# Performance work log

Hardware: AMD Instinct MI355X
Metric: run time of the kernel (lower is better)

Reference implementation:

```python
import jax, jax.numpy as jnp
import numpy as np

N = 2000
E = 20000
C = 16
B = 128
N_IN = 200   # first N_IN nodes are input nodes
N_OUT = 200  # last N_OUT nodes are output nodes
EPS = 1e-5


def setup_inputs() -> dict:
    key = jax.random.key(0)
    ks = jax.random.split(key, 8)
    x = jax.random.normal(ks[0], (B, N), dtype=jnp.float32)
    edge_index = jax.random.randint(ks[1], (2, E), 0, N, dtype=jnp.int32)
    input_node_mask = jnp.arange(N) < N_IN
    output_node_mask = jnp.arange(N) >= (N - N_OUT)
    func_mask = ~(input_node_mask | output_node_mask)
    # sparse-linear parameters (structured forms of W1/W2/W3)
    w1 = jax.random.normal(ks[2], (E, C), dtype=jnp.float32) * (1.0 / np.sqrt(C))
    b1 = jnp.zeros((N, C), dtype=jnp.float32)
    w2 = jax.random.normal(ks[3], (N, C, C), dtype=jnp.float32) * (1.0 / np.sqrt(C))
    b2 = jnp.zeros((N, C), dtype=jnp.float32)
    w3 = jax.random.normal(ks[4], (E, C), dtype=jnp.float32) * 1.0  # d=1 init scale
    b3 = jnp.zeros((E,), dtype=jnp.float32)
    g1 = jnp.ones((N * C,), dtype=jnp.float32)
    be1 = jnp.zeros((N * C,), dtype=jnp.float32)
    g2 = jnp.ones((N * C,), dtype=jnp.float32)
    be2 = jnp.zeros((N * C,), dtype=jnp.float32)
    return {"x": x, "w1": w1, "b1": b1, "w2": w2, "b2": b2, "w3": w3, "b3": b3,
            "g1": g1, "be1": be1, "g2": g2, "be2": be2,
            "edge_index": edge_index, "func_mask": func_mask,
            "output_node_mask": output_node_mask, "layers": 4}


def _batchnorm(h, g, b):
    # training-mode BatchNorm1d: batch mean and biased variance over axis 0
    m = h.mean(axis=0)
    v = h.var(axis=0)
    return (h - m) * jax.lax.rsqrt(v + EPS) * g + b


def reference(x, w1, b1, w2, b2, w3, b3, g1, be1, g2, be2,
              edge_index, func_mask, output_node_mask, layers):
    src, dst = edge_index[0], edge_index[1]
    Bsz, Nn = x.shape
    Ee, Cc = w1.shape
    fm = func_mask.astype(x.dtype)
    w2m = w2 * fm[:, None, None]          # W2 blocks exist only at function nodes
    w3m = w3 * fm[src][:, None]           # W3 rows exist only for edges with src in function nodes

    x0 = x[:, src]                        # node2edge: (B, E)
    xe = x0
    for _ in range(layers):
        # lin1: scatter edge values into dst node hidden channels
        contrib = xe.T[:, :, None] * w1[:, None, :]                    # (E, B, C)
        h = jax.ops.segment_sum(contrib, dst, num_segments=Nn)         # (N, B, C)
        h = jnp.transpose(h, (1, 0, 2)) + b1                           # (B, N, C)
        h = _batchnorm(h.reshape(Bsz, Nn * Cc), g1, be1)
        h = jax.nn.elu(h).reshape(Bsz, Nn, Cc)
        # lin2: block-diagonal C x C mix per (function) node
        h = jnp.einsum('bnc,ncd->bnd', h, w2m) + b2
        h = _batchnorm(h.reshape(Bsz, Nn * Cc), g2, be2)
        h = jax.nn.elu(h).reshape(Bsz, Nn, Cc)
        # lin3: gather src hidden, per-edge dot back to edge space
        xe = jnp.einsum('bec,ec->be', h[:, src], w3m) + b3             # (B, E)
        xe = xe + x0
    # edge2node: scatter-sum edge values to dst nodes, keep output nodes
    nodes = jax.ops.segment_sum(xe.T, dst, num_segments=Nn)            # (N, B)
    return nodes.T * output_node_mask.astype(x.dtype)
```

## Files before the change

kernel.cpp:

```cpp
#include <hip/hip_runtime.h>
#include <math.h>

#define BB 128
#define NN 2000
#define EE 20000
#define CC 16
#define FUNC_LO 200
#define FUNC_HI 1800
#define OUT_LO 1800
#define NFUNC 1600
#define NBLK 1600
#define EPSV 1e-5f
#define SS 40
#define NSLOT (NFUNC * SS)
#define HP 129

#define SCOPE_AGENT __HIP_MEMORY_SCOPE_AGENT

static __device__ __forceinline__ void xe_st(float* p, float v) {
    __hip_atomic_store(p, v, __ATOMIC_RELAXED, SCOPE_AGENT);
}

__device__ __forceinline__ void arrive(int* progress, int L) {
    asm volatile("s_waitcnt vmcnt(0)" ::: "memory");
    __syncthreads();
    if (threadIdx.x == 0)
        __hip_atomic_store(&progress[blockIdx.x], L, __ATOMIC_RELAXED, SCOPE_AGENT);
}

__device__ __forceinline__ void wait_producers(const int* progress,
                                               const int* __restrict__ pblk,
                                               int cbase, int dIn, int L) {
    if (threadIdx.x < 64) {
        int j = threadIdx.x;
        int pb = (j < dIn) ? pblk[cbase + j] : -1;
        bool done = (pb < 0);
        int tries = 0;
        while (true) {
            if (!done)
                done = (__hip_atomic_load(&progress[pb], __ATOMIC_RELAXED,
                                          SCOPE_AGENT) >= L);
            if (__ballot(!done) == 0ull) break;
            __builtin_amdgcn_s_sleep(2);
            if (++tries > (1 << 18)) break;
        }
    }
    __syncthreads();
}

#define TPB0 100
__global__ void k_prep(const float* __restrict__ x, const int* __restrict__ ei,
                       const float* __restrict__ w1, const float* __restrict__ w3,
                       const float* __restrict__ b3,
                       int* __restrict__ degIn, int* __restrict__ degF,
                       int* __restrict__ degO, int* __restrict__ posIn,
                       float* __restrict__ xT, float* __restrict__ w1s,
                       float* __restrict__ w3s, float* __restrict__ b3s,
                       int* __restrict__ inoff, int* __restrict__ wout,
                       int* __restrict__ prodBlk, float* __restrict__ out)
{
    int t = blockIdx.x * 256 + threadIdx.x;
    if (t < EE) {
        int s = ei[t], d = ei[EE + t];
        bool dFn = (d >= FUNC_LO && d < FUNC_HI);
        bool sFn = (s >= FUNC_LO && s < FUNC_HI);
        int pi = -1;
        if (dFn) {
            int p = atomicAdd(&degIn[d], 1);
            pi = (d - FUNC_LO) * SS + p;
            posIn[t] = pi;
            const float4* w1v = (const float4*)w1 + (size_t)t * 4;
            float4* w1o = (float4*)w1s + (size_t)pi * 4;
            #pragma unroll
            for (int i = 0; i < 4; i++) w1o[i] = w1v[i];
            inoff[pi] = s * BB;
            prodBlk[pi] = sFn ? (s - FUNC_LO) : (t % NBLK);
        }
        if (sFn) {
            int po = -1;
            if (dFn) {
                int q = atomicAdd(&degF[s], 1);
                po = (s - FUNC_LO) * SS + q;
                wout[po] = pi * BB;
            } else if (d >= OUT_LO) {
                int q = atomicAdd(&degO[s], 1);
                po = (s - FUNC_LO) * SS + (SS - 1 - q);
                wout[po] = d;
            }
            if (po >= 0) {
                const float4* w3v = (const float4*)w3 + (size_t)t * 4;
                float4* w3o = (float4*)w3s + (size_t)po * 4;
                #pragma unroll
                for (int i = 0; i < 4; i++) w3o[i] = w3v[i];
                b3s[po] = b3[t];
            }
        }
    }
    if (t < NN * BB) out[t] = 0.0f;

    int tb = blockIdx.x - TPB0;
    if (tb >= 0 && tb < 63 * 4) {
        __shared__ float tl[32][33];
        int ntile = tb >> 2, btile = tb & 3;
        int n0 = ntile * 32, b0 = btile * 32;
        int tx = threadIdx.x & 31, ty = threadIdx.x >> 5;
        #pragma unroll
        for (int r = 0; r < 4; r++) {
            int bb = b0 + ty * 4 + r;
            int nn2 = n0 + tx;
            tl[ty * 4 + r][tx] = (nn2 < NN) ? x[(size_t)bb * NN + nn2] : 0.0f;
        }
        __syncthreads();
        #pragma unroll
        for (int r = 0; r < 4; r++) {
            int nn2 = n0 + ty * 4 + r;
            if (nn2 < NN) xT[(size_t)nn2 * BB + b0 + tx] = tl[tx][ty * 4 + r];
        }
    }
}

__device__ __forceinline__ void bn_elu(float (&t)[CC],
                                       const float* g, const float* be,
                                       float* tile, float* part_s, float* part_ss,
                                       float* sc, float* sh, int b) {
    #pragma unroll
    for (int c = 0; c < CC; c++) tile[c * HP + b] = t[c];
    __syncthreads();
    {
        int c = b & 15, grp = b >> 4;
        float s = 0.f, ss = 0.f;
        #pragma unroll
        for (int i = 0; i < 16; i++) {
            float v = tile[c * HP + grp * 16 + i];
            s += v; ss += v * v;
        }
        part_s[grp * 16 + c] = s;
        part_ss[grp * 16 + c] = ss;
    }
    __syncthreads();
    if (b < CC) {
        float S = 0.f, SSm = 0.f;
        #pragma unroll
        for (int g8 = 0; g8 < 8; g8++) { S += part_s[g8 * 16 + b]; SSm += part_ss[g8 * 16 + b]; }
        float mean = S * (1.0f / BB);
        float var = SSm * (1.0f / BB) - mean * mean;
        float scale = rsqrtf(var + EPSV) * g[b];
        sc[b] = scale;
        sh[b] = be[b] - mean * scale;
    }
    __syncthreads();
    #pragma unroll
    for (int c = 0; c < CC; c++) {
        float u = t[c] * sc[c] + sh[c];
        t[c] = (u > 0.0f) ? u : (__expf(u) - 1.0f);
    }
}

struct FusedArgs {
    const float* xT; float* xeA; float* xeB; float* xeC;
    const float* w1s; const float* w2; const float* w3s; const float* b3s;
    const int* inoff; const int* wout; const int* prodBlk;
    const int* degIn; const int* degF; const int* degO;
    const float* g1; const float* be1; const float* g2; const float* be2;
    const int* ei; const int* posIn; const float* b3;
    float* out;
    int* progress;
};

template<bool FIRST, bool LAST>
__device__ __forceinline__ void layer_body(const FusedArgs& A,
    const float* __restrict__ xe_in, float* __restrict__ xe_out,
    int n, int b, int dIn, int dF, int dO, float x0r,
    const float* w1L, const float* w3L, const float* w2L, const float* b3L,
    const int* ioL, const int* woL,
    const float* g1L, const float* be1L, const float* g2L, const float* be2L,
    float* tile, float* part_s, float* part_ss, float* sc, float* sh)
{
    float a[CC];
    #pragma unroll
    for (int c = 0; c < CC; c++) a[c] = 0.0f;

    for (int k0 = 0; k0 < dIn; k0 += 16) {
        float v[16];
        #pragma unroll
        for (int j = 0; j < 16; j++) {
            v[j] = 0.0f;
            if (k0 + j < dIn) {
                int ro = FIRST ? ioL[k0 + j] : (k0 + j) * BB;
                v[j] = xe_in[ro + b];
            }
        }
        #pragma unroll
        for (int j = 0; j < 16; j++) {
            if (k0 + j < dIn) {
                const float* wr = &w1L[(k0 + j) * CC];
                #pragma unroll
                for (int c = 0; c < CC; c++) a[c] += v[j] * wr[c];
            }
        }
    }

    bn_elu(a, g1L, be1L, tile, part_s, part_ss, sc, sh, b);

    float h2[CC];
    #pragma unroll
    for (int d = 0; d < CC; d++) h2[d] = 0.0f;
    #pragma unroll
    for (int c = 0; c < CC; c++) {
        float av = a[c];
        #pragma unroll
        for (int d = 0; d < CC; d++) h2[d] += av * w2L[c * CC + d];
    }

    bn_elu(h2, g2L, be2L, tile, part_s, part_ss, sc, sh, b);

    if (!LAST) {
        for (int q0 = 0; q0 < dF; q0 += 4) {
            #pragma unroll
            for (int j = 0; j < 4; j++) {
                int q = q0 + j;
                if (q >= dF) break;
                const float* wr = &w3L[q * CC];
                float val = b3L[q] + x0r;
                #pragma unroll
                for (int d = 0; d < CC; d++) val += h2[d] * wr[d];
                xe_st(&xe_out[woL[q] + b], val);
            }
        }
    } else {
        for (int q0 = 0; q0 < dO; q0 += 4) {
            #pragma unroll
            for (int j = 0; j < 4; j++) {
                int q = q0 + j;
                if (q >= dO) break;
                int ql = SS - 1 - q;
                const float* wr = &w3L[ql * CC];
                float val = b3L[ql] + x0r;
                #pragma unroll
                for (int d = 0; d < CC; d++) val += h2[d] * wr[d];
                int dn = woL[ql];
                atomicAdd(&A.out[(size_t)b * NN + dn], val);
            }
        }
    }
}

__global__ __launch_bounds__(128, 4) void k_fused(FusedArgs A)
{
    const int b = threadIdx.x;
    const int blk = blockIdx.x;
    const int n = FUNC_LO + blk;
    const int cbase = blk * SS;

    __shared__ float tile[CC * HP];
    __shared__ float part_s[128], part_ss[128];
    __shared__ float sc[CC], sh[CC];
    __shared__ float w1L[SS * CC];
    __shared__ float w3L[SS * CC];
    __shared__ float w2L[CC * CC];
    __shared__ float b3L[SS];
    __shared__ int   ioL[SS];
    __shared__ int   woL[SS];
    __shared__ float g1L[CC], be1L[CC], g2L[CC], be2L[CC];

    #pragma unroll
    for (int i = b; i < SS * CC; i += 128) {
        w1L[i] = A.w1s[(size_t)cbase * CC + i];
        w3L[i] = A.w3s[(size_t)cbase * CC + i];
    }
    #pragma unroll
    for (int i = b; i < CC * CC; i += 128)
        w2L[i] = A.w2[(size_t)n * CC * CC + i];
    if (b < SS) {
        b3L[b] = A.b3s[cbase + b];
        ioL[b] = A.inoff[cbase + b];
        woL[b] = A.wout[cbase + b];
    }
    if (b < CC) {
        g1L[b] = A.g1[n * CC + b];  be1L[b] = A.be1[n * CC + b];
        g2L[b] = A.g2[n * CC + b];  be2L[b] = A.be2[n * CC + b];
    }
    const int dIn = A.degIn[n];
    const int dF  = A.degF[n];
    const int dO  = A.degO[n];
    const float x0r = A.xT[n * BB + b];

    for (int e = blk; e < EE; e += NBLK) {
        int s = A.ei[e];
        if (s >= FUNC_LO && s < FUNC_HI) continue;
        int d = A.ei[EE + e];
        float val = A.b3[e] + A.xT[s * BB + b];
        if (d >= FUNC_LO && d < FUNC_HI) {
            int ro = A.posIn[e] * BB;
            xe_st(&A.xeA[ro + b], val);
            xe_st(&A.xeB[ro + b], val);
            xe_st(&A.xeC[ro + b], val);
        } else if (d >= OUT_LO) {
            atomicAdd(&A.out[(size_t)b * NN + d], val);
        }
    }
    __syncthreads();

    const float* xeAr = A.xeA + (size_t)cbase * BB;
    const float* xeBr = A.xeB + (size_t)cbase * BB;
    const float* xeCr = A.xeC + (size_t)cbase * BB;

    layer_body<true,  false>(A, A.xT, A.xeA, n, b, dIn, dF, dO, x0r,
                             w1L, w3L, w2L, b3L, ioL, woL,
                             g1L, be1L, g2L, be2L,
                             tile, part_s, part_ss, sc, sh);
    arrive(A.progress, 1);
    wait_producers(A.progress, A.prodBlk, cbase, dIn, 1);
    layer_body<false, false>(A, xeAr, A.xeB, n, b, dIn, dF, dO, x0r,
                             w1L, w3L, w2L, b3L, ioL, woL,
                             g1L, be1L, g2L, be2L,
                             tile, part_s, part_ss, sc, sh);
    arrive(A.progress, 2);
    wait_producers(A.progress, A.prodBlk, cbase, dIn, 2);
    layer_body<false, false>(A, xeBr, A.xeC, n, b, dIn, dF, dO, x0r,
                             w1L, w3L, w2L, b3L, ioL, woL,
                             g1L, be1L, g2L, be2L,
                             tile, part_s, part_ss, sc, sh);
    arrive(A.progress, 3);
    wait_producers(A.progress, A.prodBlk, cbase, dIn, 3);
    layer_body<false, true >(A, xeCr, nullptr, n, b, dIn, dF, dO, x0r,
                             w1L, w3L, w2L, b3L, ioL, woL,
                             g1L, be1L, g2L, be2L,
                             tile, part_s, part_ss, sc, sh);
}

extern "C" void kernel_launch(void* const* d_in, const int* in_sizes, int n_in,
                              void* d_out, int out_size, void* d_ws, size_t ws_size,
                              hipStream_t stream) {
    const float* x   = (const float*)d_in[0];
    const float* w1  = (const float*)d_in[1];
    const float* w2  = (const float*)d_in[3];
    const float* w3  = (const float*)d_in[5];
    const float* b3  = (const float*)d_in[6];
    const float* g1  = (const float*)d_in[7];
    const float* be1 = (const float*)d_in[8];
    const float* g2  = (const float*)d_in[9];
    const float* be2 = (const float*)d_in[10];
    const int* ei    = (const int*)d_in[11];
    float* out = (float*)d_out;

    char* ws = (char*)d_ws;
    float* xT   = (float*)ws;  ws += (size_t)NN * BB * 4;
    float* xeA  = (float*)ws;  ws += (size_t)NSLOT * BB * 4;
    float* xeB  = (float*)ws;  ws += (size_t)NSLOT * BB * 4;
    float* xeC  = (float*)ws;  ws += (size_t)NSLOT * BB * 4;
    float* w1s  = (float*)ws;  ws += (size_t)NSLOT * CC * 4;
    float* w3s  = (float*)ws;  ws += (size_t)NSLOT * CC * 4;
    float* b3s  = (float*)ws;  ws += (size_t)NSLOT * 4;
    int* degIn  = (int*)ws;    ws += (size_t)NN * 4;
    int* degF   = (int*)ws;    ws += (size_t)NN * 4;
    int* degO   = (int*)ws;    ws += (size_t)NN * 4;
    int* progress = (int*)ws;  ws += (size_t)NBLK * 4;
    int* posIn  = (int*)ws;    ws += (size_t)EE * 4;
    int* inoff  = (int*)ws;    ws += (size_t)NSLOT * 4;
    int* wout   = (int*)ws;    ws += (size_t)NSLOT * 4;
    int* prodBlk= (int*)ws;    ws += (size_t)NSLOT * 4;

    hipMemsetAsync(degIn, 0, (3 * NN + NBLK) * sizeof(int), stream);
    k_prep<<<(NN * BB + 255) / 256, 256, 0, stream>>>(
        x, ei, w1, w3, b3, degIn, degF, degO, posIn,
        xT, w1s, w3s, b3s, inoff, wout, prodBlk, out);

    FusedArgs fa;
    fa.xT = xT; fa.xeA = xeA; fa.xeB = xeB; fa.xeC = xeC;
    fa.w1s = w1s; fa.w2 = w2; fa.w3s = w3s; fa.b3s = b3s;
    fa.inoff = inoff; fa.wout = wout; fa.prodBlk = prodBlk;
    fa.degIn = degIn; fa.degF = degF; fa.degO = degO;
    fa.g1 = g1; fa.be1 = be1; fa.g2 = g2; fa.be2 = be2;
    fa.ei = ei; fa.posIn = posIn; fa.b3 = b3;
    fa.out = out;
    fa.progress = progress;
    k_fused<<<NBLK, 128, 0, stream>>>(fa);
}
```

Baseline: 164.1 us.

## Split each node block across two thread halves to double per-node parallelism

Each node block now runs 256 threads instead of 128. The two halves of 128 take alternating incoming slots in lin1 and combine their partial sums through shared memory inside the first batchnorm. The lin3 output edges and the initial edge-scatter loop are split between the halves the same way. The aim is to shorten the serial per-thread loops over degree and hide latency with more waves, at the cost of an extra shared-memory reduction, more barriers, and tighter register limits under launch_bounds(256,7).

```diff
diff --git a/kernel.cpp b/kernel.cpp
--- a/kernel.cpp
+++ b/kernel.cpp
@@ -119,34 +119,85 @@
     }
 }
 
-__device__ __forceinline__ void bn_elu(float (&t)[CC],
-                                       const float* g, const float* be,
-                                       float* tile, float* part_s, float* part_ss,
-                                       float* sc, float* sh, int b) {
-    #pragma unroll
-    for (int c = 0; c < CC; c++) tile[c * HP + b] = t[c];
+__device__ __forceinline__ void bn_elu_partial(float (&t)[CC],
+    const float* g, const float* be,
+    float* tile, float* part_s, float* part_ss, float* sc, float* sh,
+    int b, int h, int tid)
+{
+    if (h == 1) {
+        #pragma unroll
+        for (int c = 0; c < CC; c++) tile[c * HP + b] = t[c];
+    }
+    __syncthreads();
+    if (h == 0) {
+        #pragma unroll
+        for (int c = 0; c < CC; c++) {
+            float f = t[c] + tile[c * HP + b];
+            tile[c * HP + b] = f;
+        }
+    }
     __syncthreads();
     {
-        int c = b & 15, grp = b >> 4;
+        int c = tid & 15, grp = tid >> 4;
         float s = 0.f, ss = 0.f;
         #pragma unroll
-        for (int i = 0; i < 16; i++) {
-            float v = tile[c * HP + grp * 16 + i];
+        for (int i = 0; i < 8; i++) {
+            float v = tile[c * HP + grp * 8 + i];
             s += v; ss += v * v;
         }
         part_s[grp * 16 + c] = s;
         part_ss[grp * 16 + c] = ss;
     }
     __syncthreads();
-    if (b < CC) {
+    if (tid < CC) {
         float S = 0.f, SSm = 0.f;
         #pragma unroll
-        for (int g8 = 0; g8 < 8; g8++) { S += part_s[g8 * 16 + b]; SSm += part_ss[g8 * 16 + b]; }
+        for (int g16 = 0; g16 < 16; g16++) { S += part_s[g16 * 16 + tid]; SSm += part_ss[g16 * 16 + tid]; }
         float mean = S * (1.0f / BB);
         float var = SSm * (1.0f / BB) - mean * mean;
-        float scale = rsqrtf(var + EPSV) * g[b];
-        sc[b] = scale;
-        sh[b] = be[b] - mean * scale;
+        float scale = rsqrtf(var + EPSV) * g[tid];
+        sc[tid] = scale;
+        sh[tid] = be[tid] - mean * scale;
+    }
+    __syncthreads();
+    #pragma unroll
+    for (int c = 0; c < CC; c++) {
+        float u = tile[c * HP + b] * sc[c] + sh[c];
+        t[c] = (u > 0.0f) ? u : (__expf(u) - 1.0f);
+    }
+}
+
+__device__ __forceinline__ void bn_elu_full(float (&t)[CC],
+    const float* g, const float* be,
+    float* tile, float* part_s, float* part_ss, float* sc, float* sh,
+    int b, int h, int tid)
+{
+    if (h == 0) {
+        #pragma unroll
+        for (int c = 0; c < CC; c++) tile[c * HP + b] = t[c];
+    }
+    __syncthreads();
+    {
+        int c = tid & 15, grp = tid >> 4;
+        float s = 0.f, ss = 0.f;
+        #pragma unroll
+        for (int i = 0; i < 8; i++) {
+            float v = tile[c * HP + grp * 8 + i];
+            s += v; ss += v * v;
+        }
+        part_s[grp * 16 + c] = s;
+        part_ss[grp * 16 + c] = ss;
+    }
+    __syncthreads();
+    if (tid < CC) {
+        float S = 0.f, SSm = 0.f;
+        #pragma unroll
+        for (int g16 = 0; g16 < 16; g16++) { S += part_s[g16 * 16 + tid]; SSm += part_ss[g16 * 16 + tid]; }
+        float mean = S * (1.0f / BB);
+        float var = SSm * (1.0f / BB) - mean * mean;
+        float scale = rsqrtf(var + EPSV) * g[tid];
+        sc[tid] = scale;
+        sh[tid] = be[tid] - mean * scale;
     }
     __syncthreads();
     #pragma unroll
@@ -170,7 +221,7 @@
 template<bool FIRST, bool LAST>
 __device__ __forceinline__ void layer_body(const FusedArgs& A,
     const float* __restrict__ xe_in, float* __restrict__ xe_out,
-    int n, int b, int dIn, int dF, int dO, float x0r,
+    int b, int h, int tid, int dIn, int dF, int dO, float x0r,
     const float* w1L, const float* w3L, const float* w2L, const float* b3L,
     const int* ioL, const int* woL,
     const float* g1L, const float* be1L, const float* g2L, const float* be2L,
@@ -181,26 +232,28 @@
     for (int c = 0; c < CC; c++) a[c] = 0.0f;
 
     for (int k0 = 0; k0 < dIn; k0 += 16) {
-        float v[16];
-        #pragma unroll
-        for (int j = 0; j < 16; j++) {
+        float v[8];
+        #pragma unroll
+        for (int j = 0; j < 8; j++) {
             v[j] = 0.0f;
-            if (k0 + j < dIn) {
-                int ro = FIRST ? ioL[k0 + j] : (k0 + j) * BB;
+            int sl = k0 + 2 * j + h;
+            if (sl < dIn) {
+                int ro = FIRST ? ioL[sl] : sl * BB;
                 v[j] = xe_in[ro + b];
             }
         }
         #pragma unroll
-        for (int j = 0; j < 16; j++) {
-            if (k0 + j < dIn) {
-                const float* wr = &w1L[(k0 + j) * CC];
+        for (int j = 0; j < 8; j++) {
+            int sl = k0 + 2 * j + h;
+            if (sl < dIn) {
+                const float* wr = &w1L[sl * CC];
                 #pragma unroll
                 for (int c = 0; c < CC; c++) a[c] += v[j] * wr[c];
             }
         }
     }
 
-    bn_elu(a, g1L, be1L, tile, part_s, part_ss, sc, sh, b);
+    bn_elu_partial(a, g1L, be1L, tile, part_s, part_ss, sc, sh, b, h, tid);
 
     float h2[CC];
     #pragma unroll
@@ -212,14 +265,14 @@
         for (int d = 0; d < CC; d++) h2[d] += av * w2L[c * CC + d];
     }
 
-    bn_elu(h2, g2L, be2L, tile, part_s, part_ss, sc, sh, b);
+    bn_elu_full(h2, g2L, be2L, tile, part_s, part_ss, sc, sh, b, h, tid);
 
     if (!LAST) {
-        for (int q0 = 0; q0 < dF; q0 += 4) {
+        for (int q0 = 0; q0 < dF; q0 += 8) {
             #pragma unroll
             for (int j = 0; j < 4; j++) {
-                int q = q0 + j;
-                if (q >= dF) break;
+                int q = q0 + 2 * j + h;
+                if (q >= dF) continue;
                 const float* wr = &w3L[q * CC];
                 float val = b3L[q] + x0r;
                 #pragma unroll
@@ -228,11 +281,11 @@
             }
         }
     } else {
-        for (int q0 = 0; q0 < dO; q0 += 4) {
+        for (int q0 = 0; q0 < dO; q0 += 8) {
             #pragma unroll
             for (int j = 0; j < 4; j++) {
-                int q = q0 + j;
-                if (q >= dO) break;
+                int q = q0 + 2 * j + h;
+                if (q >= dO) continue;
                 int ql = SS - 1 - q;
                 const float* wr = &w3L[ql * CC];
                 float val = b3L[ql] + x0r;
@@ -245,15 +298,17 @@
     }
 }
 
-__global__ __launch_bounds__(128, 4) void k_fused(FusedArgs A)
+__global__ __launch_bounds__(256, 7) void k_fused(FusedArgs A)
 {
-    const int b = threadIdx.x;
+    const int tid = threadIdx.x;
+    const int b = tid & (BB - 1);
+    const int h = tid >> 7;
     const int blk = blockIdx.x;
     const int n = FUNC_LO + blk;
     const int cbase = blk * SS;
 
     __shared__ float tile[CC * HP];
-    __shared__ float part_s[128], part_ss[128];
+    __shared__ float part_s[256], part_ss[256];
     __shared__ float sc[CC], sh[CC];
     __shared__ float w1L[SS * CC];
     __shared__ float w3L[SS * CC];
@@ -264,28 +319,29 @@
     __shared__ float g1L[CC], be1L[CC], g2L[CC], be2L[CC];
 
     #pragma unroll
-    for (int i = b; i < SS * CC; i += 128) {
+    for (int i = tid; i < SS * CC; i += 256) {
         w1L[i] = A.w1s[(size_t)cbase * CC + i];
         w3L[i] = A.w3s[(size_t)cbase * CC + i];
     }
-    #pragma unroll
-    for (int i = b; i < CC * CC; i += 128)
-        w2L[i] = A.w2[(size_t)n * CC * CC + i];
-    if (b < SS) {
-        b3L[b] = A.b3s[cbase + b];
-        ioL[b] = A.inoff[cbase + b];
-        woL[b] = A.wout[cbase + b];
-    }
-    if (b < CC) {
-        g1L[b] = A.g1[n * CC + b];  be1L[b] = A.be1[n * CC + b];
-        g2L[b] = A.g2[n * CC + b];  be2L[b] = A.be2[n * CC + b];
+    if (tid < CC * CC)
+        w2L[tid] = A.w2[(size_t)n * CC * CC + tid];
+    if (tid >= 256 - SS) {
+        int i = tid - (256 - SS);
+        b3L[i] = A.b3s[cbase + i];
+        ioL[i] = A.inoff[cbase + i];
+        woL[i] = A.wout[cbase + i];
+    }
+    if (tid >= 192 && tid < 192 + CC) {
+        int i = tid - 192;
+        g1L[i] = A.g1[n * CC + i];  be1L[i] = A.be1[n * CC + i];
+        g2L[i] = A.g2[n * CC + i];  be2L[i] = A.be2[n * CC + i];
     }
     const int dIn = A.degIn[n];
     const int dF  = A.degF[n];
     const int dO  = A.degO[n];
     const float x0r = A.xT[n * BB + b];
 
-    for (int e = blk; e < EE; e += NBLK) {
+    for (int e = blk + h * NBLK; e < EE; e += 2 * NBLK) {
         int s = A.ei[e];
         if (s >= FUNC_LO && s < FUNC_HI) continue;
         int d = A.ei[EE + e];
@@ -305,25 +361,25 @@
     const float* xeBr = A.xeB + (size_t)cbase * BB;
     const float* xeCr = A.xeC + (size_t)cbase * BB;
 
-    layer_body<true,  false>(A, A.xT, A.xeA, n, b, dIn, dF, dO, x0r,
+    layer_body<true,  false>(A, A.xT, A.xeA, b, h, tid, dIn, dF, dO, x0r,
                              w1L, w3L, w2L, b3L, ioL, woL,
                              g1L, be1L, g2L, be2L,
                              tile, part_s, part_ss, sc, sh);
     arrive(A.progress, 1);
     wait_producers(A.progress, A.prodBlk, cbase, dIn, 1);
-    layer_body<false, false>(A, xeAr, A.xeB, n, b, dIn, dF, dO, x0r,
+    layer_body<false, false>(A, xeAr, A.xeB, b, h, tid, dIn, dF, dO, x0r,
                              w1L, w3L, w2L, b3L, ioL, woL,
                              g1L, be1L, g2L, be2L,
                              tile, part_s, part_ss, sc, sh);
     arrive(A.progress, 2);
     wait_producers(A.progress, A.prodBlk, cbase, dIn, 2);
-    layer_body<false, false>(A, xeBr, A.xeC, n, b, dIn, dF, dO, x0r,
+    layer_body<false, false>(A, xeBr, A.xeC, b, h, tid, dIn, dF, dO, x0r,
                              w1L, w3L, w2L, b3L, ioL, woL,
                              g1L, be1L, g2L, be2L,
                              tile, part_s, part_ss, sc, sh);
     arrive(A.progress, 3);
     wait_producers(A.progress, A.prodBlk, cbase, dIn, 3);
-    layer_body<false, true >(A, xeCr, nullptr, n, b, dIn, dF, dO, x0r,
+    layer_body<false, true >(A, xeCr, nullptr, b, h, tid, dIn, dF, dO, x0r,
                              w1L, w3L, w2L, b3L, ioL, woL,
                              g1L, be1L, g2L, be2L,
                              tile, part_s, part_ss, sc, sh);
@@ -375,5 +431,5 @@
     fa.ei = ei; fa.posIn = posIn; fa.b3 = b3;
     fa.out = out;
     fa.progress = progress;
-    k_fused<<<NBLK, 128, 0, stream>>>(fa);
-}
+    k_fused<<<NBLK, 256, 0, stream>>>(fa);
+}
```

After: 172.9 us. 1.05x slower.
